# Optimization experiments

Hardware: AMD Instinct MI355X
Metric: run time of the kernel (lower is better)

## Reference

```python
import jax, jax.numpy as jnp
import numpy as np

N = 100000   # nodes per graph (protein == ligand node count, forced by cat dim=1)
E = 3200000  # edges per graph (avg degree 32)
F = 128      # input feature dim
A = 10       # action dim


def _fanin_uniform(key, shape, fanin=None):
    fanin = fanin or shape[0]
    v = 1.0 / np.sqrt(fanin)
    return jax.random.uniform(key, shape, jnp.float32, -v, v)


def setup_inputs() -> dict:
    key = jax.random.key(0)
    ks = jax.random.split(key, 24)
    inp = {
        "protein_x": jax.random.normal(ks[0], (N, F), jnp.float32),
        "protein_edges": jax.random.randint(ks[1], (2, E), 0, N, jnp.int32),
        "ligand_x": jax.random.normal(ks[2], (N, F), jnp.float32),
        "ligand_edges": jax.random.randint(ks[3], (2, E), 0, N, jnp.int32),
        "action": jax.random.normal(ks[4], (N, A), jnp.float32),
        # protein GraphConv layers
        "wp1s": _fanin_uniform(ks[5], (F, 16)),
        "wp1n": _fanin_uniform(ks[6], (F, 16)),
        "bp1": jnp.zeros((16,), jnp.float32),
        "wp2s": _fanin_uniform(ks[7], (16, 50)),
        "wp2n": _fanin_uniform(ks[8], (16, 50)),
        "bp2": jnp.zeros((50,), jnp.float32),
        # ligand GraphConv layers
        "wl1s": _fanin_uniform(ks[9], (F, 16)),
        "wl1n": _fanin_uniform(ks[10], (F, 16)),
        "bl1": jnp.zeros((16,), jnp.float32),
        "wl2s": _fanin_uniform(ks[11], (16, 50)),
        "wl2n": _fanin_uniform(ks[12], (16, 50)),
        "bl2": jnp.zeros((50,), jnp.float32),
        # MLP head
        "w_in": _fanin_uniform(ks[13], (100, 60)),
        "b_in": jnp.zeros((60,), jnp.float32),
        "w_hid": _fanin_uniform(ks[14], (60 + A, 10)),
        "b_hid": jnp.zeros((10,), jnp.float32),
        "w_out": jax.random.uniform(ks[15], (10, 1), jnp.float32, -0.003, 0.003),
        "b_out": jnp.zeros((1,), jnp.float32),
    }
    return inp


def graph_conv(x, edge_index, w_self, w_nbr, b):
    # PyG GraphConv: x_i' = x_i @ W_self + (sum_{j->i} x_j) @ W_nbr + b
    src, dst = edge_index[0], edge_index[1]
    agg = jax.ops.segment_sum(x[src], dst, num_segments=x.shape[0])  # [N, Fin]
    return x @ w_self + agg @ w_nbr + b


def reference(protein_x, protein_edges, ligand_x, ligand_edges, action,
              wp1s, wp1n, bp1, wp2s, wp2n, bp2,
              wl1s, wl1n, bl1, wl2s, wl2n, bl2,
              w_in, b_in, w_hid, b_hid, w_out, b_out):
    # protein branch (dropout is identity in eval mode)
    p = jax.nn.relu(graph_conv(protein_x, protein_edges, wp1s, wp1n, bp1))
    p = graph_conv(p, protein_edges, wp2s, wp2n, bp2)            # [N, 50]
    # ligand branch
    l = jax.nn.relu(graph_conv(ligand_x, ligand_edges, wl1s, wl1n, bl1))
    l = graph_conv(l, ligand_edges, wl2s, wl2n, bl2)             # [N, 50]
    molecule = jnp.concatenate([p, l], axis=1)                   # [N, 100]
    finger_print = jax.nn.relu(molecule @ w_in + b_in)           # [N, 60]
    policy = jnp.concatenate([finger_print, action], axis=1) @ w_hid + b_hid
    policy = jax.nn.relu(policy) @ w_out + b_out                 # [N, 1]
    return policy
```

## Files before the change

### kernel.cpp

```cpp
#include <hip/hip_runtime.h>
#include <hip/hip_bf16.h>
#include <stdint.h>


#define F_IN 128
#define NBMAX 512
#define BIN_CH 16
#define BIN_EDGES (256 * BIN_CH)
#define FINE_CAP 12288

#define OW1P  0
#define OB1P  4096
#define OW1L  4112
#define OB1L  8208
#define OC1P  8224
#define OC2P  9184
#define OC1L  10144
#define OC2L  11104
#define OBIN  12064
#define OWHID 12124
#define OBHID 12824
#define OWOUT 12834
#define OBOUT 12844
#define WBUF_FLOATS 16384

__device__ __forceinline__ float bf2f(unsigned short u) {
    union { unsigned int i; float f; } v; v.i = ((unsigned int)u) << 16; return v.f;
}
__device__ __forceinline__ float bflo(unsigned int u) {
    union { unsigned int i; float f; } v; v.i = u << 16; return v.f;
}
__device__ __forceinline__ float bfhi(unsigned int u) {
    union { unsigned int i; float f; } v; v.i = u & 0xffff0000u; return v.f;
}
__device__ __forceinline__ unsigned short f2bf(float f) {
    union { float f; unsigned int i; } v; v.f = f;
    unsigned int u = v.i;
    unsigned int r = (u + 0x7fffu + ((u >> 16) & 1u)) >> 16;
    return (unsigned short)r;
}
__device__ __forceinline__ unsigned pack2bf(float a, float b) {
    return (unsigned)f2bf(a) | ((unsigned)f2bf(b) << 16);
}
__device__ __forceinline__ float ldf(const void* p, int isf32, size_t i) {
    return isf32 ? ((const float*)p)[i] : bf2f(((const unsigned short*)p)[i]);
}

__global__ __launch_bounds__(256) void k_detect(
    const unsigned short* __restrict__ x, int nProbe, int* __restrict__ flag)
{
    __shared__ int cnt;
    if (threadIdx.x == 0) cnt = 0;
    __syncthreads();
    int bad = 0;
    for (int i = threadIdx.x; i < nProbe; i += 256) {
        unsigned e = (x[i] >> 7) & 0xFFu;
        if (e >= 140u) bad++;
    }
    atomicAdd(&cnt, bad);
    __syncthreads();
    if (threadIdx.x == 0) *flag = (cnt > nProbe / 16) ? 1 : 0;
}


struct PW {
    const void *wp1s, *wp1n, *bp1, *wl1s, *wl1n, *bl1;
    const void *wp2s, *wp2n, *bp2, *wl2s, *wl2n, *bl2;
    const void *w_in, *b_in, *w_hid, *b_hid, *w_out, *b_out;
};

__global__ __launch_bounds__(256) void k_prepw(PW P, float* __restrict__ wb,
                                               const int* __restrict__ flag)
{
    const int isf32 = *flag;
    int t = blockIdx.x * 256 + threadIdx.x;
    int stride = gridDim.x * 256;
    for (int i = t; i < 4096; i += stride) {
        int k = i >> 5, j = i & 31;
        wb[OW1P + i] = (j < 16) ? ldf(P.wp1s, isf32, k * 16 + j)
                                : ldf(P.wp1n, isf32, k * 16 + (j - 16));
        wb[OW1L + i] = (j < 16) ? ldf(P.wl1s, isf32, k * 16 + j)
                                : ldf(P.wl1n, isf32, k * 16 + (j - 16));
    }
    for (int i = t; i < 16; i += stride) {
        wb[OB1P + i] = ldf(P.bp1, isf32, i);
        wb[OB1L + i] = ldf(P.bl1, isf32, i);
    }
    for (int i = t; i < 960; i += stride) {
        int k = i / 60, j = i % 60;
        float s1 = 0.f, s2 = 0.f;
        for (int r = 0; r < 50; ++r) {
            float wi = ldf(P.w_in, isf32, r * 60 + j);
            s1 += ldf(P.wp2s, isf32, k * 50 + r) * wi;
            s2 += ldf(P.wp2n, isf32, k * 50 + r) * wi;
        }
        wb[OC1P + i] = s1; wb[OC2P + i] = s2;
    }
    for (int i = t; i < 960; i += stride) {
        int k = i / 60, j = i % 60;
        float s1 = 0.f, s2 = 0.f;
        for (int r = 0; r < 50; ++r) {
            float wi = ldf(P.w_in, isf32, (50 + r) * 60 + j);
            s1 += ldf(P.wl2s, isf32, k * 50 + r) * wi;
            s2 += ldf(P.wl2n, isf32, k * 50 + r) * wi;
        }
        wb[OC1L + i] = s1; wb[OC2L + i] = s2;
    }
    for (int i = t; i < 60; i += stride) {
        float s = ldf(P.b_in, isf32, i);
        for (int r = 0; r < 50; ++r) {
            s += ldf(P.bp2, isf32, r) * ldf(P.w_in, isf32, r * 60 + i);
            s += ldf(P.bl2, isf32, r) * ldf(P.w_in, isf32, (50 + r) * 60 + i);
        }
        wb[OBIN + i] = s;
    }
    for (int i = t; i < 700; i += stride) wb[OWHID + i] = ldf(P.w_hid, isf32, i);
    for (int i = t; i < 10; i += stride) {
        wb[OBHID + i] = ldf(P.b_hid, isf32, i);
        wb[OWOUT + i] = ldf(P.w_out, isf32, i);
    }
    if (t == 0) wb[OBOUT] = ldf(P.b_out, isf32, 0);
}


__global__ __launch_bounds__(256) void k_zero(int* __restrict__ p, int n) {
    int i = blockIdx.x * 256 + threadIdx.x;
    if (i < n) p[i] = 0;
}

__global__ __launch_bounds__(256) void k_bucket_hist(
    const int* __restrict__ ed0, const int* __restrict__ ed1,
    int* __restrict__ cnt, int nE)
{
    const int* ed = blockIdx.y ? ed1 : ed0;
    int* c = cnt + blockIdx.y * NBMAX;
    __shared__ int h[NBMAX];
    for (int i = threadIdx.x; i < NBMAX; i += 256) h[i] = 0;
    __syncthreads();
    int stride = gridDim.x * 256;
    for (int e = blockIdx.x * 256 + threadIdx.x; e < nE; e += stride)
        atomicAdd(&h[ed[e] >> 8], 1);
    __syncthreads();
    for (int i = threadIdx.x; i < NBMAX; i += 256)
        if (h[i]) atomicAdd(&c[i], h[i]);
}

__global__ __launch_bounds__(512) void k_bucket_scan(
    const int* __restrict__ cnt, int* __restrict__ base,
    int* __restrict__ cursor, int nb)
{
    const int* c = cnt + blockIdx.x * NBMAX;
    int* ba = base + blockIdx.x * 528;
    int* cu = cursor + blockIdx.x * NBMAX;
    __shared__ int sh[512];
    int t = threadIdx.x;
    int v = (t < nb) ? c[t] : 0;
    sh[t] = v;
    __syncthreads();
    for (int off = 1; off < 512; off <<= 1) {
        int x = (t >= off) ? sh[t - off] : 0;
        __syncthreads();
        sh[t] += x;
        __syncthreads();
    }
    int excl = sh[t] - v;
    if (t < nb) { ba[t] = excl; cu[t] = excl; }
    if (t == nb - 1) ba[nb] = excl + v;
}

__global__ __launch_bounds__(256) void k_bucket_bin(
    const int* __restrict__ es0, const int* __restrict__ ed0,
    const int* __restrict__ es1, const int* __restrict__ ed1,
    int* __restrict__ cursor, unsigned* __restrict__ pairs, int nE)
{
    const int* es = blockIdx.y ? es1 : es0;
    const int* ed = blockIdx.y ? ed1 : ed0;
    int* cur = cursor + blockIdx.y * NBMAX;
    unsigned* pr = pairs + (size_t)blockIdx.y * nE;

    __shared__ int h[NBMAX];
    __shared__ int lcur[NBMAX];
    __shared__ int sh[256];
    __shared__ unsigned stage[BIN_EDGES];
    __shared__ unsigned short stageB[BIN_EDGES];

    for (int i = threadIdx.x; i < NBMAX; i += 256) h[i] = 0;
    __syncthreads();
    int e0 = blockIdx.x * BIN_EDGES;
    int s[BIN_CH], d[BIN_CH];
#pragma unroll
    for (int k = 0; k < BIN_CH; ++k) {
        int e = e0 + k * 256 + threadIdx.x;
        if (e < nE) {
            s[k] = es[e]; d[k] = ed[e];
            atomicAdd(&h[d[k] >> 8], 1);
        } else d[k] = -1;
    }
    __syncthreads();
    {
        int t = threadIdx.x;
        int a = h[2 * t], b2 = h[2 * t + 1];
        sh[t] = a + b2;
        __syncthreads();
        for (int off = 1; off < 256; off <<= 1) {
            int x = (t >= off) ? sh[t - off] : 0;
            __syncthreads();
            sh[t] += x;
            __syncthreads();
        }
        int excl = sh[t] - (a + b2);
        lcur[2 * t] = excl;
        lcur[2 * t + 1] = excl + a;
    }
    __syncthreads();
    for (int b = threadIdx.x; b < NBMAX; b += 256) {
        int c = h[b];
        if (c) {
            int g = atomicAdd(&cur[b], c);
            h[b] = g - lcur[b];
        }
    }
    __syncthreads();
#pragma unroll
    for (int k = 0; k < BIN_CH; ++k) {
        if (d[k] >= 0) {
            int b = d[k] >> 8;
            int pos = atomicAdd(&lcur[b], 1);
            stage[pos] = ((unsigned)(d[k] & 255) << 24) | (unsigned)s[k];
            stageB[pos] = (unsigned short)b;
        }
    }
    __syncthreads();
    int total = nE - e0; if (total > BIN_EDGES) total = BIN_EDGES;
    for (int i = threadIdx.x; i < total; i += 256)
        pr[h[stageB[i]] + i] = stage[i];
}

__global__ __launch_bounds__(256) void k_bucket_fine(
    const unsigned* __restrict__ pairs, const int* __restrict__ base,
    int* __restrict__ row0, int* __restrict__ srcs0,
    int* __restrict__ row1, int* __restrict__ srcs1,
    int n, int nE, int nb)
{
    const unsigned* pr = pairs + (size_t)blockIdx.y * nE;
    const int* ba = base + blockIdx.y * 528;
    int* row = blockIdx.y ? row1 : row0;
    int* srcs = blockIdx.y ? srcs1 : srcs0;
    __shared__ int cnt[256], cur[256];
    __shared__ int stage[FINE_CAP];
    int b = blockIdx.x;
    int t = threadIdx.x;
    int s0 = ba[b], s1 = ba[b + 1];
    int m = s1 - s0;
    cnt[t] = 0;
    __syncthreads();
    for (int i = s0 + t; i < s1; i += 256)
        atomicAdd(&cnt[pr[i] >> 24], 1);
    __syncthreads();
    int c = cnt[t];
    cur[t] = c;
    __syncthreads();
    for (int off = 1; off < 256; off <<= 1) {
        int x = (t >= off) ? cur[t - off] : 0;
        __syncthreads();
        cur[t] += x;
        __syncthreads();
    }
    int excl = cur[t] - c;
    __syncthreads();
    int node = (b << 8) + t;
    if (node < n) row[node] = s0 + excl;
    if (b == nb - 1 && t == 0) row[n] = nE;
    if (m <= FINE_CAP) {
        cur[t] = excl;
        __syncthreads();
        for (int i = s0 + t; i < s1; i += 256) {
            unsigned p = pr[i];
            int slot = atomicAdd(&cur[p >> 24], 1);
            stage[slot] = (int)(p & 0xFFFFFFu);
        }
        __syncthreads();
        for (int i = t; i < m; i += 256)
            srcs[s0 + i] = stage[i];
    } else {
        cur[t] = s0 + excl;
        __syncthreads();
        for (int i = s0 + t; i < s1; i += 256) {
            unsigned p = pr[i];
            int slot = atomicAdd(&cur[p >> 24], 1);
            srcs[slot] = (int)(p & 0xFFFFFFu);
        }
    }
}


struct TArgs2 {
    const void* __restrict__ x;
    const float* __restrict__ w;
    const float* __restrict__ b;
    float* __restrict__ acc;
    void* __restrict__ nbr;
};

__global__ __launch_bounds__(256) void k_transform1(
    TArgs2 a0, TArgs2 a1, int n, const int* __restrict__ flag)
{
    TArgs2 A = blockIdx.y ? a1 : a0;
    const int isf32 = *flag;
    int w = threadIdx.x >> 6;
    int jh = __builtin_amdgcn_readfirstlane(w & 1);
    int node = blockIdx.x * 128 + ((w >> 1) << 6) + (threadIdx.x & 63);
    if (node >= n) return;
    const float* __restrict__ Wb = A.w + 16 * jh;
    float acc[16];
    if (jh == 0) {
#pragma unroll
        for (int j = 0; j < 16; ++j) acc[j] = A.b[j];
    } else {
#pragma unroll
        for (int j = 0; j < 16; ++j) acc[j] = 0.f;
    }

    if (isf32) {
        const float4* xr = (const float4*)((const float*)A.x + (size_t)node * F_IN);
        for (int kk = 0; kk < 32; ++kk) {
            float4 q = xr[kk];
            const float* __restrict__ w0 = Wb + kk * 128;
            float xs[4] = {q.x, q.y, q.z, q.w};
#pragma unroll
            for (int h = 0; h < 4; ++h) {
#pragma unroll
                for (int j = 0; j < 16; ++j) acc[j] += xs[h] * w0[h * 32 + j];
            }
        }
    } else {
        const uint4* xr = (const uint4*)((const unsigned short*)A.x + (size_t)node * F_IN);
        for (int kk = 0; kk < 16; ++kk) {
            uint4 q = xr[kk];
            const float* __restrict__ w0 = Wb + kk * 256;
            float xs[8] = {bflo(q.x), bfhi(q.x), bflo(q.y), bfhi(q.y),
                           bflo(q.z), bfhi(q.z), bflo(q.w), bfhi(q.w)};
#pragma unroll
            for (int h = 0; h < 8; ++h) {
#pragma unroll
                for (int j = 0; j < 16; ++j) acc[j] += xs[h] * w0[h * 32 + j];
            }
        }
    }
    if (jh == 0) {
        float4* a4 = (float4*)(A.acc + (size_t)node * 16);
#pragma unroll
        for (int t = 0; t < 4; ++t)
            a4[t] = make_float4(acc[4 * t], acc[4 * t + 1], acc[4 * t + 2], acc[4 * t + 3]);
    } else {
        unsigned short* nrow = (unsigned short*)A.nbr + ((size_t)node << 4);
        *(uint4*)nrow = make_uint4(pack2bf(acc[0], acc[1]), pack2bf(acc[2], acc[3]),
                                   pack2bf(acc[4], acc[5]), pack2bf(acc[6], acc[7]));
        *(uint4*)(nrow + 8) = make_uint4(pack2bf(acc[8], acc[9]), pack2bf(acc[10], acc[11]),
                                         pack2bf(acc[12], acc[13]), pack2bf(acc[14], acc[15]));
    }
}

struct GArgs { const int *row, *srcs; const void* val; float* out; };

__global__ __launch_bounds__(256) void k_gather16(
    GArgs g0, GArgs g1, int n, int selfmode, int yoff)
{
    GArgs G = (blockIdx.y + yoff) ? g1 : g0;
    int t = blockIdx.x * 256 + threadIdx.x;
    int node = t >> 2;
    if (node >= n) return;
    int c = (t & 3) << 2;
    const unsigned short* vb = (const unsigned short*)G.val;
    int rs = G.row[node], re = G.row[node + 1];
    float4 sum = make_float4(0.f, 0.f, 0.f, 0.f);
    if (selfmode) sum = *(const float4*)(G.out + ((size_t)node << 4) + c);
    int j = rs;
    for (; j + 8 <= re; j += 8) {
        int s[8];
        uint2 v[8];
#pragma unroll
        for (int u = 0; u < 8; ++u) s[u] = G.srcs[j + u];
#pragma unroll
        for (int u = 0; u < 8; ++u)
            v[u] = *(const uint2*)(vb + (((size_t)s[u]) << 4) + c);
#pragma unroll
        for (int u = 0; u < 8; ++u) {
            sum.x += bflo(v[u].x); sum.y += bfhi(v[u].x);
            sum.z += bflo(v[u].y); sum.w += bfhi(v[u].y);
        }
    }
    for (; j < re; ++j) {
        uint2 v = *(const uint2*)(vb + (((size_t)G.srcs[j]) << 4) + c);
        sum.x += bflo(v.x); sum.y += bfhi(v.x);
        sum.z += bflo(v.y); sum.w += bfhi(v.y);
    }
    *(float4*)(G.out + ((size_t)node << 4) + c) = sum;
}

__global__ __launch_bounds__(256) void k_relu2bf(
    const float* __restrict__ accP, const float* __restrict__ accL,
    void* __restrict__ n1P, void* __restrict__ n1L, int n)
{
    const float* a = blockIdx.y ? accL : accP;
    unsigned short* nb = (unsigned short*)(blockIdx.y ? n1L : n1P);
    int node = blockIdx.x * 256 + threadIdx.x;
    if (node >= n) return;
    const float4* r = (const float4*)(a + (size_t)node * 16);
    float p[16];
#pragma unroll
    for (int t = 0; t < 4; ++t) {
        float4 v = r[t];
        p[4 * t] = fmaxf(v.x, 0.f); p[4 * t + 1] = fmaxf(v.y, 0.f);
        p[4 * t + 2] = fmaxf(v.z, 0.f); p[4 * t + 3] = fmaxf(v.w, 0.f);
    }
    unsigned short* prow = nb + ((size_t)node << 4);
    *(uint4*)prow = make_uint4(pack2bf(p[0], p[1]), pack2bf(p[2], p[3]),
                               pack2bf(p[4], p[5]), pack2bf(p[6], p[7]));
    *(uint4*)(prow + 8) = make_uint4(pack2bf(p[8], p[9]), pack2bf(p[10], p[11]),
                                     pack2bf(p[12], p[13]), pack2bf(p[14], p[15]));
}

__device__ __forceinline__ void fp_acc30(float* fp, const float* __restrict__ wb,
                                         int off, int jo,
                                         const float* __restrict__ row, bool dorelu)
{
    const float4* r4 = (const float4*)row;
    for (int kk = 0; kk < 4; ++kk) {
        float4 v = r4[kk];
        float xs[4] = {v.x, v.y, v.z, v.w};
        if (dorelu) {
            xs[0] = fmaxf(xs[0], 0.f); xs[1] = fmaxf(xs[1], 0.f);
            xs[2] = fmaxf(xs[2], 0.f); xs[3] = fmaxf(xs[3], 0.f);
        }
        const float* __restrict__ wq = wb + off + kk * 240 + jo;
#pragma unroll
        for (int h = 0; h < 4; ++h) {
#pragma unroll
            for (int j = 0; j < 30; ++j) fp[j] += xs[h] * wq[h * 60 + j];
        }
    }
}

__global__ __launch_bounds__(256) void k_headf(
    const float* __restrict__ hP, const float* __restrict__ gP,
    const float* __restrict__ hL, const float* __restrict__ gL,
    const void* __restrict__ action, const float* __restrict__ wb,
    void* __restrict__ out, int n, const int* __restrict__ flag)
{
    const int isf32 = *flag;
    __shared__ float hbuf[128][10];
    int w = threadIdx.x >> 6;
    int jh = __builtin_amdgcn_readfirstlane(w & 1);
    int slot = ((w >> 1) << 6) + (threadIdx.x & 63);
    int node = blockIdx.x * 128 + slot;
    int nodec = node < n ? node : (n - 1);
    const int jo = 30 * jh;

    float fp[30];
#pragma unroll
    for (int j = 0; j < 30; ++j) fp[j] = wb[OBIN + jo + j];

    fp_acc30(fp, wb, OC1P, jo, hP + (size_t)nodec * 16, true);
    fp_acc30(fp, wb, OC2P, jo, gP + (size_t)nodec * 16, false);
    fp_acc30(fp, wb, OC1L, jo, hL + (size_t)nodec * 16, true);
    fp_acc30(fp, wb, OC2L, jo, gL + (size_t)nodec * 16, false);

    float h[10];
#pragma unroll
    for (int j = 0; j < 10; ++j) h[j] = (jh == 0) ? wb[OBHID + j] : 0.f;
#pragma unroll
    for (int k = 0; k < 30; ++k) {
        float v = fmaxf(fp[k], 0.f);
#pragma unroll
        for (int j = 0; j < 10; ++j) h[j] += v * wb[OWHID + (jo + k) * 10 + j];
    }
    if (jh) {
#pragma unroll
        for (int j = 0; j < 10; ++j) hbuf[slot][j] = h[j];
    }
    __syncthreads();
    if (jh == 0) {
#pragma unroll
        for (int j = 0; j < 10; ++j) h[j] += hbuf[slot][j];
#pragma unroll
        for (int k = 0; k < 10; ++k) {
            float v = ldf(action, isf32, (size_t)nodec * 10 + k);
#pragma unroll
            for (int j = 0; j < 10; ++j) h[j] += v * wb[OWHID + (60 + k) * 10 + j];
        }
        float o = wb[OBOUT];
#pragma unroll
        for (int j = 0; j < 10; ++j) o += fmaxf(h[j], 0.f) * wb[OWOUT + j];
        if (node < n) {
            if (isf32) ((float*)out)[node] = o;
            else       ((unsigned short*)out)[node] = f2bf(o);
        }
    }
}

extern "C" void kernel_launch(void* const* d_in, const int* in_sizes, int n_in,
                              void* d_out, int out_size, void* d_ws, size_t ws_size,
                              hipStream_t stream)
{
    const void* px   = d_in[0];
    const int*  pe   = (const int*)d_in[1];
    const void* lx   = d_in[2];
    const int*  le   = (const int*)d_in[3];
    const void* act  = d_in[4];

    const int N = in_sizes[0] / F_IN;
    const int E = in_sizes[1] / 2;
    const int NB = (N + 255) >> 8;

    int* flag    = (int*)d_ws;
    int* cnt     = flag + 64;
    int* base    = cnt + 2 * NBMAX;
    int* cursorB = base + 2 * 528;
    float* wbuf  = (float*)(flag + 3200);
    int* rowP    = flag + 3200 + WBUF_FLOATS;
    int* srcsP   = rowP + (N + 64);
    int* rowL    = srcsP + E;
    int* srcsL   = rowL + (N + 64);
    float* dense = (float*)(srcsL + E);
    unsigned* pairs = (unsigned*)dense;

    float* accP = dense;
    float* accL = accP + (size_t)N * 16;
    float* aggP = accL + (size_t)N * 16;
    float* aggL = aggP + (size_t)N * 16;
    void*  n1P  = (void*)(aggL + (size_t)N * 16);
    void*  n1L  = (void*)((float*)n1P + (size_t)N * 8);

    const int nb = (N + 255) / 256;
    const int nb2 = (N + 127) / 128;
    const int gb = (N * 4 + 255) / 256;
    const int bb = (E + BIN_EDGES - 1) / BIN_EDGES;

    k_detect<<<1, 256, 0, stream>>>((const unsigned short*)px, 4096, flag);

    PW P{d_in[5], d_in[6], d_in[7], d_in[11], d_in[12], d_in[13],
         d_in[8], d_in[9], d_in[10], d_in[14], d_in[15], d_in[16],
         d_in[17], d_in[18], d_in[19], d_in[20], d_in[21], d_in[22]};
    k_prepw<<<32, 256, 0, stream>>>(P, wbuf, flag);

    k_zero<<<4, 256, 0, stream>>>(cnt, 2 * NBMAX);
    k_bucket_hist<<<dim3(512, 2), 256, 0, stream>>>(pe + E, le + E, cnt, E);
    k_bucket_scan<<<2, 512, 0, stream>>>(cnt, base, cursorB, NB);
    k_bucket_bin<<<dim3(bb, 2), 256, 0, stream>>>(pe, pe + E, le, le + E,
                                                  cursorB, pairs, E);
    k_bucket_fine<<<dim3(NB, 2), 256, 0, stream>>>(pairs, base, rowP, srcsP,
                                                   rowL, srcsL, N, E, NB);

    TArgs2 tP{px, wbuf + OW1P, wbuf + OB1P, accP, n1P};
    TArgs2 tL{lx, wbuf + OW1L, wbuf + OB1L, accL, n1L};
    k_transform1<<<dim3(nb2, 2), 256, 0, stream>>>(tP, tL, N, flag);

    GArgs g1P{rowP, srcsP, n1P, accP}, g1L{rowL, srcsL, n1L, accL};
    k_gather16<<<gb, 256, 0, stream>>>(g1P, g1L, N, 1, 0);
    k_gather16<<<gb, 256, 0, stream>>>(g1P, g1L, N, 1, 1);

    k_relu2bf<<<dim3(nb, 2), 256, 0, stream>>>(accP, accL, n1P, n1L, N);

    GArgs g2P{rowP, srcsP, n1P, aggP}, g2L{rowL, srcsL, n1L, aggL};
    k_gather16<<<gb, 256, 0, stream>>>(g2P, g2L, N, 0, 0);
    k_gather16<<<gb, 256, 0, stream>>>(g2P, g2L, N, 0, 1);

    k_headf<<<nb2, 256, 0, stream>>>(accP, aggP, accL, aggL, act, wbuf,
                                     d_out, N, flag);
}
```

Baseline: 524.2 us.

## Stage transform1 input tile in LDS and fuse ReLU/bf16 pack into gather

k_transform1 now loads each 128-node feature tile cooperatively into a 64KB XOR-swizzled shared-memory buffer, so the two waves that compute the two output halves share a single global read instead of each reading the row. The separate k_relu2bf kernel is removed. The first-layer gather now also writes the ReLU'd bf16 rows into new n2P/n2L buffers, which avoids a kernel launch and a full re-read of the accumulators. The 64KB of LDS per block may limit occupancy, and the extra buffers enlarge the workspace footprint.

```diff
diff --git a/kernel.cpp b/kernel.cpp
--- a/kernel.cpp
+++ b/kernel.cpp
@@ -307,11 +307,43 @@
 {
     TArgs2 A = blockIdx.y ? a1 : a0;
     const int isf32 = *flag;
-    int w = threadIdx.x >> 6;
-    int jh = __builtin_amdgcn_readfirstlane(w & 1);
-    int node = blockIdx.x * 128 + ((w >> 1) << 6) + (threadIdx.x & 63);
+    __shared__ unsigned char xs_raw[65536];
+    const int t = threadIdx.x;
+    const int tile0 = blockIdx.x * 128;
+
+    if (isf32) {
+        const float4* xg = (const float4*)A.x;
+        float4* xl = (float4*)xs_raw;
+#pragma unroll
+        for (int i = 0; i < 16; ++i) {
+            int flat = i * 256 + t;
+            int row = flat >> 5, ck = flat & 31;
+            if (tile0 + row < n)
+                xl[row * 32 + (ck ^ (row & 7))] =
+                    xg[((size_t)(tile0 + row)) * 32 + ck];
+        }
+    } else {
+        const uint4* xg = (const uint4*)A.x;
+        uint4* xl = (uint4*)xs_raw;
+#pragma unroll
+        for (int i = 0; i < 8; ++i) {
+            int flat = i * 256 + t;
+            int row = flat >> 4, ck = flat & 15;
+            if (tile0 + row < n)
+                xl[row * 16 + (ck ^ (row & 7))] =
+                    xg[((size_t)(tile0 + row)) * 16 + ck];
+        }
+    }
+    __syncthreads();
+
+    const int w = t >> 6;
+    const int jh = __builtin_amdgcn_readfirstlane(w >> 1);
+    const int r = ((w & 1) << 6) + (t & 63);
+    const int node = tile0 + r;
     if (node >= n) return;
     const float* __restrict__ Wb = A.w + 16 * jh;
+    const int sw = r & 7;
+
     float acc[16];
     if (jh == 0) {
 #pragma unroll
@@ -322,36 +354,38 @@
     }
 
     if (isf32) {
-        const float4* xr = (const float4*)((const float*)A.x + (size_t)node * F_IN);
+        const float4* xl = (const float4*)xs_raw + r * 32;
         for (int kk = 0; kk < 32; ++kk) {
-            float4 q = xr[kk];
-            const float* __restrict__ w0 = Wb + kk * 128;
-            float xs[4] = {q.x, q.y, q.z, q.w};
+            float4 q = xl[kk ^ sw];
+            float xv[4] = {q.x, q.y, q.z, q.w};
 #pragma unroll
             for (int h = 0; h < 4; ++h) {
-#pragma unroll
-                for (int j = 0; j < 16; ++j) acc[j] += xs[h] * w0[h * 32 + j];
+                const float* __restrict__ w0 = Wb + (kk * 4 + h) * 32;
+#pragma unroll
+                for (int j = 0; j < 16; ++j) acc[j] += xv[h] * w0[j];
             }
         }
     } else {
-        const uint4* xr = (const uint4*)((const unsigned short*)A.x + (size_t)node * F_IN);
+        const uint4* xl = (const uint4*)xs_raw + r * 16;
         for (int kk = 0; kk < 16; ++kk) {
-            uint4 q = xr[kk];
-            const float* __restrict__ w0 = Wb + kk * 256;
-            float xs[8] = {bflo(q.x), bfhi(q.x), bflo(q.y), bfhi(q.y),
+            uint4 q = xl[kk ^ sw];
+            float xv[8] = {bflo(q.x), bfhi(q.x), bflo(q.y), bfhi(q.y),
                            bflo(q.z), bfhi(q.z), bflo(q.w), bfhi(q.w)};
 #pragma unroll
             for (int h = 0; h < 8; ++h) {
-#pragma unroll
-                for (int j = 0; j < 16; ++j) acc[j] += xs[h] * w0[h * 32 + j];
+                const float* __restrict__ w0 = Wb + (kk * 8 + h) * 32;
+#pragma unroll
+                for (int j = 0; j < 16; ++j) acc[j] += xv[h] * w0[j];
             }
         }
     }
+
     if (jh == 0) {
         float4* a4 = (float4*)(A.acc + (size_t)node * 16);
 #pragma unroll
-        for (int t = 0; t < 4; ++t)
-            a4[t] = make_float4(acc[4 * t], acc[4 * t + 1], acc[4 * t + 2], acc[4 * t + 3]);
+        for (int q = 0; q < 4; ++q)
+            a4[q] = make_float4(acc[4 * q], acc[4 * q + 1],
+                                acc[4 * q + 2], acc[4 * q + 3]);
     } else {
         unsigned short* nrow = (unsigned short*)A.nbr + ((size_t)node << 4);
         *(uint4*)nrow = make_uint4(pack2bf(acc[0], acc[1]), pack2bf(acc[2], acc[3]),
@@ -361,7 +395,7 @@
     }
 }
 
-struct GArgs { const int *row, *srcs; const void* val; float* out; };
+struct GArgs { const int *row, *srcs; const void* val; float* out; void* rout; };
 
 __global__ __launch_bounds__(256) void k_gather16(
     GArgs g0, GArgs g1, int n, int selfmode, int yoff)
@@ -396,29 +430,11 @@
         sum.z += bflo(v.y); sum.w += bfhi(v.y);
     }
     *(float4*)(G.out + ((size_t)node << 4) + c) = sum;
-}
-
-__global__ __launch_bounds__(256) void k_relu2bf(
-    const float* __restrict__ accP, const float* __restrict__ accL,
-    void* __restrict__ n1P, void* __restrict__ n1L, int n)
-{
-    const float* a = blockIdx.y ? accL : accP;
-    unsigned short* nb = (unsigned short*)(blockIdx.y ? n1L : n1P);
-    int node = blockIdx.x * 256 + threadIdx.x;
-    if (node >= n) return;
-    const float4* r = (const float4*)(a + (size_t)node * 16);
-    float p[16];
-#pragma unroll
-    for (int t = 0; t < 4; ++t) {
-        float4 v = r[t];
-        p[4 * t] = fmaxf(v.x, 0.f); p[4 * t + 1] = fmaxf(v.y, 0.f);
-        p[4 * t + 2] = fmaxf(v.z, 0.f); p[4 * t + 3] = fmaxf(v.w, 0.f);
-    }
-    unsigned short* prow = nb + ((size_t)node << 4);
-    *(uint4*)prow = make_uint4(pack2bf(p[0], p[1]), pack2bf(p[2], p[3]),
-                               pack2bf(p[4], p[5]), pack2bf(p[6], p[7]));
-    *(uint4*)(prow + 8) = make_uint4(pack2bf(p[8], p[9]), pack2bf(p[10], p[11]),
-                                     pack2bf(p[12], p[13]), pack2bf(p[14], p[15]));
+    if (selfmode) {
+        unsigned short* orow = (unsigned short*)G.rout + ((size_t)node << 4) + c;
+        *(uint2*)orow = make_uint2(pack2bf(fmaxf(sum.x, 0.f), fmaxf(sum.y, 0.f)),
+                                   pack2bf(fmaxf(sum.z, 0.f), fmaxf(sum.w, 0.f)));
+    }
 }
 
 __device__ __forceinline__ void fp_acc30(float* fp, const float* __restrict__ wb,
@@ -531,8 +547,9 @@
     float* aggL = aggP + (size_t)N * 16;
     void*  n1P  = (void*)(aggL + (size_t)N * 16);
     void*  n1L  = (void*)((float*)n1P + (size_t)N * 8);
-
-    const int nb = (N + 255) / 256;
+    void*  n2P  = (void*)((float*)n1L + (size_t)N * 8);
+    void*  n2L  = (void*)((float*)n2P + (size_t)N * 8);
+
     const int nb2 = (N + 127) / 128;
     const int gb = (N * 4 + 255) / 256;
     const int bb = (E + BIN_EDGES - 1) / BIN_EDGES;
@@ -556,13 +573,11 @@
     TArgs2 tL{lx, wbuf + OW1L, wbuf + OB1L, accL, n1L};
     k_transform1<<<dim3(nb2, 2), 256, 0, stream>>>(tP, tL, N, flag);
 
-    GArgs g1P{rowP, srcsP, n1P, accP}, g1L{rowL, srcsL, n1L, accL};
+    GArgs g1P{rowP, srcsP, n1P, accP, n2P}, g1L{rowL, srcsL, n1L, accL, n2L};
     k_gather16<<<gb, 256, 0, stream>>>(g1P, g1L, N, 1, 0);
     k_gather16<<<gb, 256, 0, stream>>>(g1P, g1L, N, 1, 1);
 
-    k_relu2bf<<<dim3(nb, 2), 256, 0, stream>>>(accP, accL, n1P, n1L, N);
-
-    GArgs g2P{rowP, srcsP, n1P, aggP}, g2L{rowL, srcsL, n1L, aggL};
+    GArgs g2P{rowP, srcsP, n2P, aggP, nullptr}, g2L{rowL, srcsL, n2L, aggL, nullptr};
     k_gather16<<<gb, 256, 0, stream>>>(g2P, g2L, N, 0, 0);
     k_gather16<<<gb, 256, 0, stream>>>(g2P, g2L, N, 0, 1);
 
```

Result: no change. 526.4 us (+0.4%).
